# Kernel optimization log

Measured on AMD Instinct MI355X. Metric: run time of the kernel, lower is better.

Reference implementation:

```python
import jax, jax.numpy as jnp
import numpy as np


def _conv1x1(x, w, b):
    # 1x1 conv == pointwise channel matmul. x:[n,c,h,w], w:[o,c], b:[o]
    return jnp.einsum('nchw,oc->nohw', x, w) + b[None, :, None, None]


def _route_gates(x, w1, b1, w2, b2):
    # Conv2d(4,2,1) -> AdaptiveAvgPool2d(1) -> Conv2d(2,2,1), flattened to [n,2].
    # 1x1 conv is pointwise-linear, so it commutes with the spatial mean:
    # mean(conv1(x)) == conv1(mean(x)). Pool first to avoid an [n,2,h,w] temp.
    p = x.mean(axis=(2, 3))            # [n, 4]
    g = p @ w1.T + b1                  # [n, 2]
    g = g @ w2.T + b2                  # [n, 2]
    return g


def setup_inputs() -> dict:
    key = jax.random.key(0)
    ks = jax.random.split(key, 16)
    N, C, H, W = 64, 4, 256, 256

    def u(k, shape, fan_in):
        bound = 1.0 / np.sqrt(fan_in)
        return jax.random.uniform(k, shape, jnp.float32, -bound, bound)

    return {
        'x': jax.random.normal(ks[0], (N, C, H, W), jnp.float32),
        'y': jax.random.normal(ks[1], (N, C, H, W), jnp.float32),
        # route_func params (shared between x and y paths, like self.route_func)
        'w_rf1': u(ks[2], (2, 4), 4), 'b_rf1': u(ks[3], (2,), 4),
        'w_rf2': u(ks[4], (2, 2), 2), 'b_rf2': u(ks[5], (2,), 2),
        # experts (1x1 convs)
        'w_e1': u(ks[6], (4, 4), 4), 'b_e1': u(ks[7], (4,), 4),
        'w_e2': u(ks[8], (8, 4), 4), 'b_e2': u(ks[9], (8,), 4),
        'w_e3': u(ks[10], (4, 4), 4), 'b_e3': u(ks[11], (4,), 4),
        'w_e4': u(ks[12], (8, 4), 4), 'b_e4': u(ks[13], (8,), 4),
    }


def reference(x, y, w_rf1, b_rf1, w_rf2, b_rf2,
              w_e1, b_e1, w_e2, b_e2, w_e3, b_e3, w_e4, b_e4):
    # Annotator([0]) only tags the batch dim: mathematically identity.
    gx = _route_gates(x, w_rf1, b_rf1, w_rf2, b_rf2)   # [n, 2]
    gy = _route_gates(y, w_rf1, b_rf1, w_rf2, b_rf2)   # [n, 2]

    # Threshold protocol (threshold=0): sample n goes to branch i iff gate[n,i] > 0.
    # Dispatch fabric scatters the selected samples to the expert; combine fabric
    # gathers expert outputs back to original batch slots (zeros where not routed).
    # This is mathematically: mask_i * expert_i(input), summed across routers.
    dt = x.dtype
    mx0 = (gx[:, 0] > 0).astype(dt)[:, None, None, None]
    mx1 = (gx[:, 1] > 0).astype(dt)[:, None, None, None]
    my0 = (gy[:, 0] > 0).astype(dt)[:, None, None, None]
    my1 = (gy[:, 1] > 0).astype(dt)[:, None, None, None]

    out_x = mx0 * _conv1x1(x, w_e1, b_e1) + my0 * _conv1x1(y, w_e3, b_e3)  # [n,4,h,w]
    out_y = mx1 * _conv1x1(x, w_e2, b_e2) + my1 * _conv1x1(y, w_e4, b_e4)  # [n,8,h,w]
    return (out_x, out_y)
```

## Files before the change

kernel.cpp:

```cpp
#include <hip/hip_runtime.h>

#define HW   65536
#define HW4  16384
#define NC   256
#define NB   64

typedef float vf4 __attribute__((ext_vector_type(4)));

__global__ void __launch_bounds__(256)
partial_sum_kernel(const float* __restrict__ x, const float* __restrict__ y,
                   float* __restrict__ partials) {
    const int blk   = blockIdx.x;
    const int plane = blk >> 2;
    const int q     = blk & 3;
    const float* src = (plane < NC) ? x : y;
    const int p = plane & (NC - 1);
    const vf4* base = (const vf4*)(src + (size_t)p * HW) + q * 4096;

    float s = 0.f;
    #pragma unroll
    for (int it = 0; it < 4; ++it) {
        int i = it * 1024 + threadIdx.x;
        vf4 v0 = base[i];
        vf4 v1 = base[i + 256];
        vf4 v2 = base[i + 512];
        vf4 v3 = base[i + 768];
        s += (v0.x + v0.y) + (v0.z + v0.w);
        s += (v1.x + v1.y) + (v1.z + v1.w);
        s += (v2.x + v2.y) + (v2.z + v2.w);
        s += (v3.x + v3.y) + (v3.z + v3.w);
    }
    #pragma unroll
    for (int off = 32; off > 0; off >>= 1)
        s += __shfl_down(s, off);
    __shared__ float ls[4];
    const int lane = threadIdx.x & 63, wv = threadIdx.x >> 6;
    if (lane == 0) ls[wv] = s;
    __syncthreads();
    if (threadIdx.x == 0)
        partials[blk] = (ls[0] + ls[1]) + (ls[2] + ls[3]);
}

__global__ void __launch_bounds__(256)
main_kernel(const float* __restrict__ x, const float* __restrict__ y,
            const float* __restrict__ partials,
            const float* __restrict__ w1, const float* __restrict__ b1,
            const float* __restrict__ w2, const float* __restrict__ b2,
            const float* __restrict__ we1, const float* __restrict__ be1,
            const float* __restrict__ we2, const float* __restrict__ be2,
            const float* __restrict__ we3, const float* __restrict__ be3,
            const float* __restrict__ we4, const float* __restrict__ be4,
            float* __restrict__ outx, float* __restrict__ outy) {
    const int blk   = blockIdx.x;
    const int n     = blk >> 6;
    const int chunk = blk & 63;
    const int hw4   = chunk * 256 + threadIdx.x;

    const float inv = 1.0f / (float)HW;
    float g[2][2];
    #pragma unroll
    for (int t = 0; t < 2; ++t) {
        float p[4];
        #pragma unroll
        for (int c = 0; c < 4; ++c) {
            const float* pp = partials + (t * NC + n * 4 + c) * 4;
            p[c] = ((pp[0] + pp[1]) + (pp[2] + pp[3])) * inv;
        }
        float h0 = w1[0]*p[0] + w1[1]*p[1] + w1[2]*p[2] + w1[3]*p[3] + b1[0];
        float h1 = w1[4]*p[0] + w1[5]*p[1] + w1[6]*p[2] + w1[7]*p[3] + b1[1];
        g[t][0] = w2[0]*h0 + w2[1]*h1 + b2[0];
        g[t][1] = w2[2]*h0 + w2[3]*h1 + b2[1];
    }
    const float mx0 = g[0][0] > 0.f ? 1.f : 0.f;
    const float mx1 = g[0][1] > 0.f ? 1.f : 0.f;
    const float my0 = g[1][0] > 0.f ? 1.f : 0.f;
    const float my1 = g[1][1] > 0.f ? 1.f : 0.f;

    const vf4* xb = (const vf4*)(x + (size_t)n * 4 * HW);
    const vf4* yb = (const vf4*)(y + (size_t)n * 4 * HW);

    vf4 xv[4] = {}, yv[4] = {};
    if (mx0 + mx1 > 0.f) {
        #pragma unroll
        for (int c = 0; c < 4; ++c) xv[c] = xb[c * HW4 + hw4];
    }
    if (my0 + my1 > 0.f) {
        #pragma unroll
        for (int c = 0; c < 4; ++c) yv[c] = yb[c * HW4 + hw4];
    }

    vf4* ox = (vf4*)(outx + (size_t)n * 4 * HW);
    #pragma unroll
    for (int o = 0; o < 4; ++o) {
        const float bb = mx0 * be1[o] + my0 * be3[o];
        vf4 a = {bb, bb, bb, bb};
        #pragma unroll
        for (int c = 0; c < 4; ++c) {
            const float wx = mx0 * we1[o * 4 + c];
            const float wy = my0 * we3[o * 4 + c];
            a += wx * xv[c] + wy * yv[c];
        }
        __builtin_nontemporal_store(a, &ox[o * HW4 + hw4]);
    }

    vf4* oy = (vf4*)(outy + (size_t)n * 8 * HW);
    #pragma unroll
    for (int o = 0; o < 8; ++o) {
        const float bb = mx1 * be2[o] + my1 * be4[o];
        vf4 a = {bb, bb, bb, bb};
        #pragma unroll
        for (int c = 0; c < 4; ++c) {
            const float wx = mx1 * we2[o * 4 + c];
            const float wy = my1 * we4[o * 4 + c];
            a += wx * xv[c] + wy * yv[c];
        }
        __builtin_nontemporal_store(a, &oy[o * HW4 + hw4]);
    }
}

extern "C" void kernel_launch(void* const* d_in, const int* in_sizes, int n_in,
                              void* d_out, int out_size, void* d_ws, size_t ws_size,
                              hipStream_t stream) {
    const float* x     = (const float*)d_in[0];
    const float* y     = (const float*)d_in[1];
    const float* w_rf1 = (const float*)d_in[2];
    const float* b_rf1 = (const float*)d_in[3];
    const float* w_rf2 = (const float*)d_in[4];
    const float* b_rf2 = (const float*)d_in[5];
    const float* w_e1  = (const float*)d_in[6];
    const float* b_e1  = (const float*)d_in[7];
    const float* w_e2  = (const float*)d_in[8];
    const float* b_e2  = (const float*)d_in[9];
    const float* w_e3  = (const float*)d_in[10];
    const float* b_e3  = (const float*)d_in[11];
    const float* w_e4  = (const float*)d_in[12];
    const float* b_e4  = (const float*)d_in[13];

    float* ws       = (float*)d_ws;
    float* partials = ws;

    float* outx = (float*)d_out;
    float* outy = outx + (size_t)NB * 4 * HW;

    hipLaunchKernelGGL(partial_sum_kernel, dim3(2048), dim3(256), 0, stream,
                       x, y, partials);
    hipLaunchKernelGGL(main_kernel, dim3(4096), dim3(256), 0, stream,
                       x, y, partials,
                       w_rf1, b_rf1, w_rf2, b_rf2,
                       w_e1, b_e1, w_e2, b_e2, w_e3, b_e3, w_e4, b_e4,
                       outx, outy);
}
```

Before: 331.9 us.

## Fuse gate reduction and expert compute into one cooperative kernel with grid sync

Replaces the two-pass launch with a single cooperative kernel. Each block reduces its slice for the per-channel means while holding y tiles in registers, then grid-syncs, computes the gates and writes the outputs. Only x is re-read after the sync. This is meant to remove the second full read of y and one kernel launch. It adds the cost of a grid-wide barrier and higher register pressure, and it falls back to the old path if the cooperative launch fails.

Result: slower. 488.9 us (+47.3%).

```diff
diff --git a/kernel.cpp b/kernel.cpp
--- a/kernel.cpp
+++ b/kernel.cpp
@@ -1,4 +1,7 @@
 #include <hip/hip_runtime.h>
+#include <hip/hip_cooperative_groups.h>
+
+namespace cg = cooperative_groups;
 
 #define HW   65536
 #define HW4  16384
@@ -6,6 +9,122 @@
 #define NB   64
 
 typedef float vf4 __attribute__((ext_vector_type(4)));
+
+__global__ void __launch_bounds__(256, 4)
+fused_kernel(const float* __restrict__ x, const float* __restrict__ y,
+             float* __restrict__ partials,
+             const float* __restrict__ w1, const float* __restrict__ b1,
+             const float* __restrict__ w2, const float* __restrict__ b2,
+             const float* __restrict__ we1, const float* __restrict__ be1,
+             const float* __restrict__ we2, const float* __restrict__ be2,
+             const float* __restrict__ we3, const float* __restrict__ be3,
+             const float* __restrict__ we4, const float* __restrict__ be4,
+             float* __restrict__ outx, float* __restrict__ outy)
+{
+    const int b  = blockIdx.x;
+    const int n  = b >> 4;
+    const int kb = b & 15;
+    const int t  = threadIdx.x;
+
+    const vf4* xb = (const vf4*)(x + (size_t)n * 4 * HW);
+    const vf4* yb = (const vf4*)(y + (size_t)n * 4 * HW);
+
+    vf4 yr[4][4];
+    float xs[4] = {0.f, 0.f, 0.f, 0.f};
+    float ys[4] = {0.f, 0.f, 0.f, 0.f};
+
+    #pragma unroll
+    for (int k = 0; k < 4; ++k) {
+        const int hw4 = (kb * 4 + k) * 256 + t;
+        #pragma unroll
+        for (int c = 0; c < 4; ++c) {
+            vf4 xv = xb[c * HW4 + hw4];
+            vf4 yv = yb[c * HW4 + hw4];
+            yr[k][c] = yv;
+            xs[c] += (xv.x + xv.y) + (xv.z + xv.w);
+            ys[c] += (yv.x + yv.y) + (yv.z + yv.w);
+        }
+    }
+
+    #pragma unroll
+    for (int off = 32; off > 0; off >>= 1) {
+        #pragma unroll
+        for (int c = 0; c < 4; ++c) {
+            xs[c] += __shfl_down(xs[c], off);
+            ys[c] += __shfl_down(ys[c], off);
+        }
+    }
+    __shared__ float ls[4][8];
+    const int lane = t & 63, wv = t >> 6;
+    if (lane == 0) {
+        #pragma unroll
+        for (int c = 0; c < 4; ++c) { ls[wv][c] = xs[c]; ls[wv][4 + c] = ys[c]; }
+    }
+    __syncthreads();
+    if (t < 8) {
+        const float v = (ls[0][t] + ls[1][t]) + (ls[2][t] + ls[3][t]);
+        const int tt = t >> 2;
+        const int c  = t & 3;
+        partials[((tt * NB + n) * 4 + c) * 16 + kb] = v;
+    }
+
+    cg::this_grid().sync();
+
+    const float inv = 1.0f / (float)HW;
+    float g[2][2];
+    #pragma unroll
+    for (int tt = 0; tt < 2; ++tt) {
+        float p[4];
+        #pragma unroll
+        for (int c = 0; c < 4; ++c) {
+            const float* pp = partials + ((tt * NB + n) * 4 + c) * 16;
+            float s0 = 0.f;
+            #pragma unroll
+            for (int k2 = 0; k2 < 16; ++k2) s0 += pp[k2];
+            p[c] = s0 * inv;
+        }
+        float h0 = w1[0]*p[0] + w1[1]*p[1] + w1[2]*p[2] + w1[3]*p[3] + b1[0];
+        float h1 = w1[4]*p[0] + w1[5]*p[1] + w1[6]*p[2] + w1[7]*p[3] + b1[1];
+        g[tt][0] = w2[0]*h0 + w2[1]*h1 + b2[0];
+        g[tt][1] = w2[2]*h0 + w2[3]*h1 + b2[1];
+    }
+    const float mx0 = g[0][0] > 0.f ? 1.f : 0.f;
+    const float mx1 = g[0][1] > 0.f ? 1.f : 0.f;
+    const float my0 = g[1][0] > 0.f ? 1.f : 0.f;
+    const float my1 = g[1][1] > 0.f ? 1.f : 0.f;
+    const bool needx = (mx0 + mx1) > 0.f;
+
+    vf4* ox = (vf4*)(outx + (size_t)n * 4 * HW);
+    vf4* oy = (vf4*)(outy + (size_t)n * 8 * HW);
+
+    #pragma unroll
+    for (int k = 0; k < 4; ++k) {
+        const int hw4 = (kb * 4 + k) * 256 + t;
+        vf4 xv[4] = {};
+        if (needx) {
+            #pragma unroll
+            for (int c = 0; c < 4; ++c) xv[c] = xb[c * HW4 + hw4];
+        }
+        #pragma unroll
+        for (int o = 0; o < 4; ++o) {
+            const float bb = mx0 * be1[o] + my0 * be3[o];
+            vf4 a = {bb, bb, bb, bb};
+            #pragma unroll
+            for (int c = 0; c < 4; ++c)
+                a += (mx0 * we1[o * 4 + c]) * xv[c] + (my0 * we3[o * 4 + c]) * yr[k][c];
+            __builtin_nontemporal_store(a, &ox[o * HW4 + hw4]);
+        }
+        #pragma unroll
+        for (int o = 0; o < 8; ++o) {
+            const float bb = mx1 * be2[o] + my1 * be4[o];
+            vf4 a = {bb, bb, bb, bb};
+            #pragma unroll
+            for (int c = 0; c < 4; ++c)
+                a += (mx1 * we2[o * 4 + c]) * xv[c] + (my1 * we4[o * 4 + c]) * yr[k][c];
+            __builtin_nontemporal_store(a, &oy[o * HW4 + hw4]);
+        }
+    }
+}
 
 __global__ void __launch_bounds__(256)
 partial_sum_kernel(const float* __restrict__ x, const float* __restrict__ y,
@@ -102,7 +221,6 @@
         }
         __builtin_nontemporal_store(a, &ox[o * HW4 + hw4]);
     }
-
     vf4* oy = (vf4*)(outy + (size_t)n * 8 * HW);
     #pragma unroll
     for (int o = 0; o < 8; ++o) {
@@ -136,17 +254,33 @@
     const float* w_e4  = (const float*)d_in[12];
     const float* b_e4  = (const float*)d_in[13];
 
-    float* ws       = (float*)d_ws;
-    float* partials = ws;
+    float* partials = (float*)d_ws;
 
     float* outx = (float*)d_out;
     float* outy = outx + (size_t)NB * 4 * HW;
 
-    hipLaunchKernelGGL(partial_sum_kernel, dim3(2048), dim3(256), 0, stream,
-                       x, y, partials);
-    hipLaunchKernelGGL(main_kernel, dim3(4096), dim3(256), 0, stream,
-                       x, y, partials,
-                       w_rf1, b_rf1, w_rf2, b_rf2,
-                       w_e1, b_e1, w_e2, b_e2, w_e3, b_e3, w_e4, b_e4,
-                       outx, outy);
-}
+    const float* ax = x;  const float* ay = y;  float* ap = partials;
+    const float* a1 = w_rf1; const float* a2 = b_rf1;
+    const float* a3 = w_rf2; const float* a4 = b_rf2;
+    const float* a5 = w_e1;  const float* a6 = b_e1;
+    const float* a7 = w_e2;  const float* a8 = b_e2;
+    const float* a9 = w_e3;  const float* aA = b_e3;
+    const float* aB = w_e4;  const float* aC = b_e4;
+    float* aX = outx; float* aY = outy;
+    void* args[] = {&ax, &ay, &ap, &a1, &a2, &a3, &a4,
+                    &a5, &a6, &a7, &a8, &a9, &aA, &aB, &aC, &aX, &aY};
+
+    hipError_t e = hipLaunchCooperativeKernel((const void*)fused_kernel,
+                                              dim3(1024), dim3(256),
+                                              args, 0, stream);
+    if (e != hipSuccess) {
+        (void)hipGetLastError();
+        hipLaunchKernelGGL(partial_sum_kernel, dim3(2048), dim3(256), 0, stream,
+                           x, y, partials);
+        hipLaunchKernelGGL(main_kernel, dim3(4096), dim3(256), 0, stream,
+                           x, y, partials,
+                           w_rf1, b_rf1, w_rf2, b_rf2,
+                           w_e1, b_e1, w_e2, b_e2, w_e3, b_e3, w_e4, b_e4,
+                           outx, outy);
+    }
+}
```
